# Kernel optimization log

Measured on AMD Instinct MI355X. Metric: run time of the kernel, lower is better.

The kernel has to match this reference:

```python
import jax, jax.numpy as jnp
import numpy as np

N = 8192      # batched tree nodes
HD = 1024     # head_dim
D = 1024      # input_dim == output_dim


def _xavier(key, shape):
    fan_out, fan_in = shape
    std = (2.0 / (fan_in + fan_out)) ** 0.5
    return std * jax.random.normal(key, shape, dtype=jnp.float32)


def setup_inputs() -> dict:
    key = jax.random.key(0)
    ks = jax.random.split(key, 16)
    inp = {
        "x_l": jax.random.normal(ks[0], (N, HD), jnp.float32),
        "h_l": jax.random.normal(ks[1], (N, D), jnp.float32),
        "c_l": jax.random.normal(ks[2], (N, D), jnp.float32),
        "x_r": jax.random.normal(ks[3], (N, HD), jnp.float32),
        "h_r": jax.random.normal(ks[4], (N, D), jnp.float32),
        "c_r": jax.random.normal(ks[5], (N, D), jnp.float32),
        # Linear weights stored torch-style [out, in]; biases init to 0 per reset_parameters
        "W_i": _xavier(ks[6], (D, 4 * D)),   "b_i": jnp.zeros((D,), jnp.float32),
        "W_fl": _xavier(ks[7], (D, 4 * D)),  "b_fl": jnp.zeros((D,), jnp.float32),
        "W_fr": _xavier(ks[8], (D, 4 * D)),  "b_fr": jnp.zeros((D,), jnp.float32),
        "W_xin": _xavier(ks[9], (4 * D, HD)),
        "W_o": _xavier(ks[10], (D, 3 * D)),  "b_o": jnp.zeros((D,), jnp.float32),
        "W_z": _xavier(ks[11], (HD, 2 * HD)), "b_z": jnp.zeros((HD,), jnp.float32),
        "W_g": _xavier(ks[12], (D, 2 * D)),  "b_g": jnp.zeros((D,), jnp.float32),
        "dim": 1,
    }
    return inp


def reference(x_l, h_l, c_l, x_r, h_r, c_r,
              W_i, b_i, W_fl, b_fl, W_fr, b_fr, W_xin,
              W_o, b_o, W_z, b_z, W_g, b_g, dim):
    lin = lambda x, W, b: x @ W.T + b
    # gating to merge child head representations
    child_x = jnp.concatenate([x_l, x_r], axis=dim)
    z_t = jax.nn.sigmoid(lin(child_x, W_z, b_z))
    x_t = z_t * x_l + (1.0 - z_t) * x_r
    # input projection (no bias), split into 4 gates
    x_in_t = x_t @ W_xin.T                      # [N, 4D]
    x_i, x_f, x_o, x_g = jnp.split(x_in_t, 4, axis=dim)
    concat_input = jnp.concatenate([h_l, h_r, c_l, c_r], axis=dim)  # [N, 4D]
    i_t = jax.nn.sigmoid(lin(concat_input, W_i, b_i) + x_i)
    f_lt = jax.nn.sigmoid(lin(concat_input, W_fl, b_fl) + x_f)
    f_rt = jax.nn.sigmoid(lin(concat_input, W_fr, b_fr) + x_f)
    concat_g = jnp.concatenate([h_l, h_r], axis=dim)
    g_t = jnp.tanh(x_g + lin(concat_g, W_g, b_g))  # dropout p=0 -> identity
    c_t = f_lt * c_l + f_rt * c_r + i_t * g_t
    concat_o = jnp.concatenate([h_l, h_r, c_t], axis=dim)
    o_t = jax.nn.sigmoid(x_o + lin(concat_o, W_o, b_o))
    h_t = o_t * jnp.tanh(c_t)
    return (x_t, h_t, c_t)
```

## Files before the change

### kernel.cpp

```cpp
#include <hip/hip_runtime.h>
#include <math.h>

#define NROWS 8192

typedef __attribute__((ext_vector_type(4))) float f32x4;
typedef __attribute__((ext_vector_type(4))) int i32x4;

__device__ __forceinline__ unsigned short f2bf(float f) {
  union { float f; unsigned int u; } v; v.f = f;
  unsigned int u = v.u;
  unsigned int r = (u + 0x7fffu + ((u >> 16) & 1u)) >> 16;
  return (unsigned short)r;
}
__device__ __forceinline__ float bf2f(unsigned short h) {
  union { unsigned int u; float f; } v; v.u = ((unsigned int)h) << 16;
  return v.f;
}
__device__ __forceinline__ float sigmoidf_(float x) { return 1.0f / (1.0f + expf(-x)); }

#define SA_INV   21.1666667f
#define SW3_INV  1016.0f
#define SWZ_INV  793.75f
#define SC_PRE3  4.64876e-5f
#define SC_ZG    5.95201e-5f

__device__ __forceinline__ unsigned char q8(float x, float inv) {
  float v = fminf(fmaxf(x * inv, -127.f), 127.f);
  return (unsigned char)(signed char)(int)rintf(v);
}

#define FENCE __builtin_amdgcn_sched_barrier(0)
#define BAR   __builtin_amdgcn_s_barrier()
#define WAIT_VM4  do { asm volatile("s_waitcnt vmcnt(4)" ::: "memory"); } while (0)
#define WAIT_VM0  do { asm volatile("s_waitcnt vmcnt(0)" ::: "memory"); } while (0)

#define LA8(buf, h) (((buf) * 4 + (h)) * 16384)
#define LB8(buf, h) (((buf) * 4 + 2 + (h)) * 16384)

#define GEMM_CORE8                                                              \
  __shared__ unsigned char lds8[131072];                                        \
  const int tid  = threadIdx.x;                                                 \
  const int wave = tid >> 6;                                                    \
  const int lane = tid & 63;                                                    \
  const int wm = wave >> 2;                                                     \
  const int wn = wave & 3;                                                      \
  const int lr = lane & 15;                                                     \
  const int kq = lane >> 4;                                                     \
  const int rsub = lane >> 3;                                                   \
  const int usw  = (lane & 7) ^ rsub;                                           \
  const int swz = (bid & 7) * (nwg >> 3) + (bid >> 3);                          \
  const int brow = (swz / nbx) * 256;                                           \
  const int bcol = (swz % nbx) * 256;                                           \
  const int nkt = K >> 7;                                                       \
  const int niter = K >> 8;                                                     \
  i32x4 acc[8][4];                                                              \
  _Pragma("unroll")                                                             \
  for (int m = 0; m < 8; ++m)                                                   \
    _Pragma("unroll")                                                           \
    for (int n = 0; n < 4; ++n)                                                 \
      acc[m][n] = (i32x4){0, 0, 0, 0};                                          \
  auto STAGE = [&](const unsigned char* src, int ld, int rowbase, int base_b,   \
                   int kt) {                                                    \
    const int k0 = (kt < nkt) ? (kt << 7) : 0;                                  \
    _Pragma("unroll")                                                           \
    for (int j = 0; j < 2; ++j) {                                               \
      const int chunk = wave * 2 + j;                                           \
      const unsigned char* g =                                                  \
          src + (size_t)(rowbase + chunk * 8 + rsub) * ld + k0 + usw * 16;      \
      __builtin_amdgcn_global_load_lds(                                         \
          (const __attribute__((address_space(1))) void*)g,                     \
          (__attribute__((address_space(3))) void*)&lds8[base_b + chunk * 1024],\
          16, 0, 0);                                                            \
    }                                                                           \
  };                                                                            \
  i32x4 aM[8], aM2[8], bN[4];                                                   \
  auto LDA_ = [&](int buf, int mh, i32x4* d) {                                  \
    _Pragma("unroll")                                                           \
    for (int m = 0; m < 4; ++m)                                                 \
      _Pragma("unroll")                                                         \
      for (int kk = 0; kk < 2; ++kk) {                                          \
        const int r = mh * 64 + m * 16 + lr;                                    \
        const int u = (kk * 4 + kq) ^ (lr & 7);                                 \
        d[m * 2 + kk] = *(const i32x4*)&lds8[LA8(buf, wm) + r * 128 + u * 16];  \
      }                                                                         \
  };                                                                            \
  auto LDB_ = [&](int buf, int nh, i32x4* d) {                                  \
    _Pragma("unroll")                                                           \
    for (int n = 0; n < 2; ++n)                                                 \
      _Pragma("unroll")                                                         \
      for (int kk = 0; kk < 2; ++kk) {                                          \
        const int r = (wn & 1) * 64 + nh * 32 + n * 16 + lr;                    \
        const int u = (kk * 4 + kq) ^ (lr & 7);                                 \
        d[n * 2 + kk] =                                                         \
            *(const i32x4*)&lds8[LB8(buf, wn >> 1) + r * 128 + u * 16];         \
      }                                                                         \
  };                                                                            \
  auto MM_ = [&](int mh, int nh, i32x4* a, i32x4* b) {                          \
    _Pragma("unroll")                                                           \
    for (int m = 0; m < 4; ++m)                                                 \
      _Pragma("unroll")                                                         \
      for (int n = 0; n < 2; ++n)                                               \
        _Pragma("unroll")                                                       \
        for (int kk = 0; kk < 2; ++kk)                                          \
          acc[mh * 4 + m][nh * 2 + n] =                                         \
              __builtin_amdgcn_mfma_i32_16x16x64_i8(                            \
                  a[m * 2 + kk], b[n * 2 + kk], acc[mh * 4 + m][nh * 2 + n],    \
                  0, 0, 0);                                                     \
  };                                                                            \
  STAGE(A, lda, brow,       LA8(0, 0), 0);                                      \
  STAGE(A, lda, brow + 128, LA8(0, 1), 0);                                      \
  STAGE(B, ldb, bcol,       LB8(0, 0), 0);                                      \
  STAGE(B, ldb, bcol + 128, LB8(0, 1), 0);                                      \
  STAGE(A, lda, brow,       LA8(1, 0), 1);                                      \
  STAGE(A, lda, brow + 128, LA8(1, 1), 1);                                      \
  WAIT_VM4; FENCE; BAR;                                                         \
  for (int i = 0; i < niter; ++i) {                                             \
    const int t1 = 2 * i + 1, t2 = 2 * i + 2, t3 = 2 * i + 3;                   \
    LDB_(0, 0, bN); LDA_(0, 0, aM); LDA_(0, 1, aM2);                            \
    STAGE(B, ldb, bcol,       LB8(1, 0), t1);                                   \
    STAGE(B, ldb, bcol + 128, LB8(1, 1), t1);                                   \
    FENCE; BAR; FENCE;                                                          \
    __builtin_amdgcn_s_setprio(1);                                              \
    MM_(0, 0, aM, bN); MM_(1, 0, aM2, bN);                                      \
    __builtin_amdgcn_s_setprio(0);                                              \
    FENCE; BAR;                                                                 \
    LDB_(0, 1, bN);                                                             \
    STAGE(A, lda, brow,       LA8(0, 0), t2);                                   \
    STAGE(A, lda, brow + 128, LA8(0, 1), t2);                                   \
    FENCE; BAR; FENCE;                                                          \
    __builtin_amdgcn_s_setprio(1);                                              \
    MM_(0, 1, aM, bN); MM_(1, 1, aM2, bN);                                      \
    __builtin_amdgcn_s_setprio(0);                                              \
    WAIT_VM4; FENCE; BAR;                                                       \
    LDB_(1, 0, bN); LDA_(1, 0, aM); LDA_(1, 1, aM2);                            \
    STAGE(B, ldb, bcol,       LB8(0, 0), t2);                                   \
    STAGE(B, ldb, bcol + 128, LB8(0, 1), t2);                                   \
    FENCE; BAR; FENCE;                                                          \
    __builtin_amdgcn_s_setprio(1);                                              \
    MM_(0, 0, aM, bN); MM_(1, 0, aM2, bN);                                      \
    __builtin_amdgcn_s_setprio(0);                                              \
    FENCE; BAR;                                                                 \
    LDB_(1, 1, bN);                                                             \
    STAGE(A, lda, brow,       LA8(1, 0), t3);                                   \
    STAGE(A, lda, brow + 128, LA8(1, 1), t3);                                   \
    FENCE; BAR; FENCE;                                                          \
    __builtin_amdgcn_s_setprio(1);                                              \
    MM_(0, 1, aM, bN); MM_(1, 1, aM2, bN);                                      \
    __builtin_amdgcn_s_setprio(0);                                              \
    WAIT_VM4; FENCE; BAR;                                                       \
  }                                                                             \
  WAIT_VM0;                                                                     \
  const int crow0 = brow + wm * 128 + kq * 4;                                   \
  const int ccol0 = bcol + wn * 64 + lr;

__global__ __launch_bounds__(512) void gemm_ACg8(
    const unsigned char* __restrict__ A3i, const unsigned char* __restrict__ W3q,
    unsigned short* __restrict__ pre3,
    const unsigned char* __restrict__ Wgq, unsigned short* __restrict__ preg,
    const unsigned char* __restrict__ A1q, const unsigned char* __restrict__ WbZq,
    unsigned short* __restrict__ zpre)
{
  const int b = (int)blockIdx.x;
  const unsigned char* A;
  const unsigned char* B;
  unsigned short* Cb;
  int K, lda, ldb, ldc, nbx, nwg, bid;
  float cscale;
  if (b < 384) {
    A = A3i; B = W3q; Cb = pre3; K = 4096; lda = 4096; ldb = 4096; ldc = 3072;
    nbx = 12; nwg = 384; bid = b; cscale = SC_PRE3;
  } else if (b < 512) {
    A = A3i; B = Wgq; Cb = preg; K = 2048; lda = 4096; ldb = 2048; ldc = 1024;
    nbx = 4; nwg = 128; bid = b - 384; cscale = SC_ZG;
  } else {
    A = A1q; B = WbZq; Cb = zpre; K = 2048; lda = 2048; ldb = 2048; ldc = 1024;
    nbx = 4; nwg = 128; bid = b - 512; cscale = SC_ZG;
  }
  GEMM_CORE8
#pragma unroll
  for (int mi = 0; mi < 8; ++mi)
#pragma unroll
    for (int ni = 0; ni < 4; ++ni)
#pragma unroll
      for (int j = 0; j < 4; ++j)
        Cb[(size_t)(crow0 + mi * 16 + j) * ldc + ccol0 + ni * 16] =
            f2bf((float)acc[mi][ni][j] * cscale);
}

__global__ __launch_bounds__(512) void gemm_B8(
    const unsigned char* __restrict__ A2q, const unsigned char* __restrict__ Wxq,
    unsigned short* __restrict__ xin)
{
  const int K = 1024, lda = 1024, ldb = 1024, ldc = 4096, nbx = 16;
  const int nwg = (int)gridDim.x;
  const int bid = (int)blockIdx.x;
  const unsigned char* A = A2q;
  const unsigned char* B = Wxq;
  GEMM_CORE8
#pragma unroll
  for (int mi = 0; mi < 8; ++mi)
#pragma unroll
    for (int ni = 0; ni < 4; ++ni)
#pragma unroll
      for (int j = 0; j < 4; ++j)
        xin[(size_t)(crow0 + mi * 16 + j) * ldc + ccol0 + ni * 16] =
            f2bf((float)acc[mi][ni][j] * SC_PRE3);
}

__global__ __launch_bounds__(512) void gemm_D8(
    const unsigned char* __restrict__ A3i, const unsigned char* __restrict__ Woq,
    unsigned short* __restrict__ opre0, unsigned short* __restrict__ opre1)
{
  const int b = (int)blockIdx.x;
  const bool sec = (b >= 128);
  const unsigned char* A = A3i + (sec ? 1536 : 0);
  const unsigned char* B = Woq + (sec ? 1536 : 0);
  unsigned short* Cb = sec ? opre1 : opre0;
  const int K = 1536, lda = 4096, ldb = 3072, ldc = 1024, nbx = 4, nwg = 128;
  const int bid = sec ? b - 128 : b;
  GEMM_CORE8
#pragma unroll
  for (int mi = 0; mi < 8; ++mi)
#pragma unroll
    for (int ni = 0; ni < 4; ++ni)
#pragma unroll
      for (int j = 0; j < 4; ++j)
        Cb[(size_t)(crow0 + mi * 16 + j) * ldc + ccol0 + ni * 16] =
            f2bf((float)acc[mi][ni][j] * SC_ZG);
}

#define NB_WZ 2048
#define NB_W3 12288
#define NB_WG 2048
#define NB_A1 16384
#define NB_A3 32768

__global__ void prep_kernel(unsigned char* __restrict__ WbZq, const float* __restrict__ W_z,
                            unsigned char* __restrict__ W3q,
                            const float* __restrict__ Wi, const float* __restrict__ Wfl,
                            const float* __restrict__ Wfr,
                            unsigned char* __restrict__ Wgq, const float* __restrict__ Wg,
                            unsigned char* __restrict__ A1q,
                            const float* __restrict__ x_l, const float* __restrict__ x_r,
                            unsigned short* __restrict__ Ac,
                            unsigned char* __restrict__ A3i,
                            const float* __restrict__ h_l, const float* __restrict__ h_r,
                            const float* __restrict__ c_l, const float* __restrict__ c_r)
{
  int b = (int)blockIdx.x;
  if (b < NB_WZ) {
    size_t idx = ((size_t)b * 256 + threadIdx.x) * 4;
    float4 v = *(const float4*)&W_z[idx];
    uchar4 q;
    q.x = q8(v.x, SWZ_INV); q.y = q8(v.y, SWZ_INV);
    q.z = q8(v.z, SWZ_INV); q.w = q8(v.w, SWZ_INV);
    *(uchar4*)&WbZq[idx] = q;
  } else if (b < NB_WZ + NB_W3) {
    size_t idx = ((size_t)(b - NB_WZ) * 256 + threadIdx.x) * 4;
    int m = (int)(idx >> 12);
    int k = (int)(idx & 4095);
    const float* W = (m < 1024) ? Wi : (m < 2048) ? Wfl : Wfr;
    float4 v = *(const float4*)&W[(size_t)(m & 1023) * 4096 + k];
    uchar4 q;
    q.x = q8(v.x, SW3_INV); q.y = q8(v.y, SW3_INV);
    q.z = q8(v.z, SW3_INV); q.w = q8(v.w, SW3_INV);
    *(uchar4*)&W3q[idx] = q;
  } else if (b < NB_WZ + NB_W3 + NB_WG) {
    size_t idx = ((size_t)(b - NB_WZ - NB_W3) * 256 + threadIdx.x) * 4;
    float4 v = *(const float4*)&Wg[idx];
    uchar4 q;
    q.x = q8(v.x, SWZ_INV); q.y = q8(v.y, SWZ_INV);
    q.z = q8(v.z, SWZ_INV); q.w = q8(v.w, SWZ_INV);
    *(uchar4*)&Wgq[idx] = q;
  } else if (b < NB_WZ + NB_W3 + NB_WG + NB_A1) {
    size_t idx = ((size_t)(b - NB_WZ - NB_W3 - NB_WG) * 256 + threadIdx.x) * 4;
    size_t n = idx >> 11;
    int rem = (int)(idx & 2047);
    const float* s = (rem < 1024) ? x_l : x_r;
    float4 v = *(const float4*)&s[(n << 10) + (rem & 1023)];
    uchar4 q;
    q.x = q8(v.x, SA_INV); q.y = q8(v.y, SA_INV);
    q.z = q8(v.z, SA_INV); q.w = q8(v.w, SA_INV);
    *(uchar4*)&A1q[idx] = q;
  } else {
    size_t idx = ((size_t)(b - NB_WZ - NB_W3 - NB_WG - NB_A1) * 256 + threadIdx.x) * 4;
    size_t n = idx >> 12;
    int rem = (int)(idx & 4095);
    int i = rem >> 10;
    int j = rem & 1023;
    const float* s = (i == 0) ? h_l : (i == 1) ? h_r : (i == 2) ? c_l : c_r;
    float4 v = *(const float4*)&s[(n << 10) + j];
    uchar4 q;
    q.x = q8(v.x, SA_INV); q.y = q8(v.y, SA_INV);
    q.z = q8(v.z, SA_INV); q.w = q8(v.w, SA_INV);
    *(uchar4*)&A3i[idx] = q;
    if (i >= 2) {
      ushort4 o;
      o.x = f2bf(v.x); o.y = f2bf(v.y); o.z = f2bf(v.z); o.w = f2bf(v.w);
      *(ushort4*)&Ac[n * 2048 + (i - 2) * 1024 + j] = o;
    }
  }
}

#define NB_EW1 8192
__global__ void ew1wx_kernel(const unsigned short* __restrict__ zp,
                             const float* __restrict__ bz,
                             const float* __restrict__ xl, const float* __restrict__ xr,
                             float* __restrict__ out_x, unsigned char* __restrict__ A2q,
                             unsigned char* __restrict__ Wxq, const float* __restrict__ W_xin)
{
  int b = (int)blockIdx.x;
  if (b < NB_EW1) {
    size_t idx = ((size_t)b * 256 + threadIdx.x) * 4;
    int j = (int)(idx & 1023);
    ushort4 z4 = *(const ushort4*)&zp[idx];
    float4 bz4 = *(const float4*)&bz[j];
    float4 xl4 = *(const float4*)&xl[idx];
    float4 xr4 = *(const float4*)&xr[idx];
    float4 xo;
    uchar4 aq;
    float z, xt;
    z = sigmoidf_(bf2f(z4.x) + bz4.x); xt = z * xl4.x + (1.f - z) * xr4.x; xo.x = xt; aq.x = q8(xt, SA_INV);
    z = sigmoidf_(bf2f(z4.y) + bz4.y); xt = z * xl4.y + (1.f - z) * xr4.y; xo.y = xt; aq.y = q8(xt, SA_INV);
    z = sigmoidf_(bf2f(z4.z) + bz4.z); xt = z * xl4.z + (1.f - z) * xr4.z; xo.z = xt; aq.z = q8(xt, SA_INV);
    z = sigmoidf_(bf2f(z4.w) + bz4.w); xt = z * xl4.w + (1.f - z) * xr4.w; xo.w = xt; aq.w = q8(xt, SA_INV);
    *(float4*)&out_x[idx] = xo;
    *(uchar4*)&A2q[idx] = aq;
  } else {
    size_t idx = ((size_t)(b - NB_EW1) * 256 + threadIdx.x) * 4;
    float4 v = *(const float4*)&W_xin[idx];
    uchar4 q;
    q.x = q8(v.x, SW3_INV); q.y = q8(v.y, SW3_INV);
    q.z = q8(v.z, SW3_INV); q.w = q8(v.w, SW3_INV);
    *(uchar4*)&Wxq[idx] = q;
  }
}

#define NB_EW2 8192
__global__ void ew2wo_kernel(const unsigned short* __restrict__ pre3,
                             const unsigned short* __restrict__ preg,
                             const unsigned short* __restrict__ xin,
                             const float* __restrict__ b_i, const float* __restrict__ b_fl,
                             const float* __restrict__ b_fr, const float* __restrict__ b_g,
                             float* __restrict__ out_c, unsigned short* __restrict__ Ac,
                             unsigned char* __restrict__ A3i,
                             unsigned char* __restrict__ Woq, const float* __restrict__ W_o)
{
  int b = (int)blockIdx.x;
  if (b < NB_EW2) {
    size_t idx = ((size_t)b * 256 + threadIdx.x) * 4;
    int j = (int)(idx & 1023);
    size_t n = idx >> 10;
    size_t r3 = n * 3072;
    size_t r4 = n << 12;
    size_t r2 = n << 11;
    ushort4 pi = *(const ushort4*)&pre3[r3 + j];
    ushort4 pf1 = *(const ushort4*)&pre3[r3 + 1024 + j];
    ushort4 pf2 = *(const ushort4*)&pre3[r3 + 2048 + j];
    ushort4 pg = *(const ushort4*)&preg[idx];
    ushort4 xi = *(const ushort4*)&xin[r4 + j];
    ushort4 xf = *(const ushort4*)&xin[r4 + 1024 + j];
    ushort4 xg = *(const ushort4*)&xin[r4 + 3072 + j];
    ushort4 cl4 = *(const ushort4*)&Ac[r2 + j];
    ushort4 cr4 = *(const ushort4*)&Ac[r2 + 1024 + j];
    float4 bi4 = *(const float4*)&b_i[j];
    float4 bfl4 = *(const float4*)&b_fl[j];
    float4 bfr4 = *(const float4*)&b_fr[j];
    float4 bg4 = *(const float4*)&b_g[j];
    float4 co;
    ushort4 ao;
    uchar4 aq;
#define EW2_ONE(pi_, pf1_, pf2_, pg_, xi_, xf_, xg_, bi_, bfl_, bfr_, bg_, cl_, cr_, oc_, oa_, oq_) \
    { float xiv = bf2f(xi_), xfv = bf2f(xf_), xgv = bf2f(xg_);                                      \
      float it = sigmoidf_(bf2f(pi_) + bi_ + xiv);                                                  \
      float fl = sigmoidf_(bf2f(pf1_) + bfl_ + xfv);                                                \
      float fr = sigmoidf_(bf2f(pf2_) + bfr_ + xfv);                                                \
      float g  = tanhf(bf2f(pg_) + bg_ + xgv);                                                      \
      float c_ = fl * bf2f(cl_) + fr * bf2f(cr_) + it * g;                                          \
      oc_ = c_; oa_ = f2bf(c_); oq_ = q8(c_, SA_INV); }
    EW2_ONE(pi.x, pf1.x, pf2.x, pg.x, xi.x, xf.x, xg.x, bi4.x, bfl4.x, bfr4.x, bg4.x, cl4.x, cr4.x, co.x, ao.x, aq.x)
    EW2_ONE(pi.y, pf1.y, pf2.y, pg.y, xi.y, xf.y, xg.y, bi4.y, bfl4.y, bfr4.y, bg4.y, cl4.y, cr4.y, co.y, ao.y, aq.y)
    EW2_ONE(pi.z, pf1.z, pf2.z, pg.z, xi.z, xf.z, xg.z, bi4.z, bfl4.z, bfr4.z, bg4.z, cl4.z, cr4.z, co.z, ao.z, aq.z)
    EW2_ONE(pi.w, pf1.w, pf2.w, pg.w, xi.w, xf.w, xg.w, bi4.w, bfl4.w, bfr4.w, bg4.w, cl4.w, cr4.w, co.w, ao.w, aq.w)
#undef EW2_ONE
    *(float4*)&out_c[idx] = co;
    *(ushort4*)&Ac[r2 + j] = ao;
    *(uchar4*)&A3i[r4 + 2048 + j] = aq;
  } else {
    size_t idx = ((size_t)(b - NB_EW2) * 256 + threadIdx.x) * 4;
    float4 v = *(const float4*)&W_o[idx];
    uchar4 q;
    q.x = q8(v.x, SWZ_INV); q.y = q8(v.y, SWZ_INV);
    q.z = q8(v.z, SWZ_INV); q.w = q8(v.w, SWZ_INV);
    *(uchar4*)&Woq[idx] = q;
  }
}

__global__ void ew3_kernel(const unsigned short* __restrict__ op0,
                           const unsigned short* __restrict__ op1,
                           const float* __restrict__ b_o,
                           const unsigned short* __restrict__ xin,
                           const unsigned short* __restrict__ Ac,
                           float* __restrict__ out_h)
{
  size_t idx = ((size_t)blockIdx.x * 256 + threadIdx.x) * 4;
  int j = (int)(idx & 1023);
  size_t n = idx >> 10;
  ushort4 opa = *(const ushort4*)&op0[idx];
  ushort4 opb = *(const ushort4*)&op1[idx];
  ushort4 xo = *(const ushort4*)&xin[(n << 12) + 2048 + j];
  ushort4 ct4 = *(const ushort4*)&Ac[(n << 11) + j];
  float4 bo4 = *(const float4*)&b_o[j];
  float4 ho;
  ho.x = sigmoidf_(bf2f(opa.x) + bf2f(opb.x) + bo4.x + bf2f(xo.x)) * tanhf(bf2f(ct4.x));
  ho.y = sigmoidf_(bf2f(opa.y) + bf2f(opb.y) + bo4.y + bf2f(xo.y)) * tanhf(bf2f(ct4.y));
  ho.z = sigmoidf_(bf2f(opa.z) + bf2f(opb.z) + bo4.z + bf2f(xo.z)) * tanhf(bf2f(ct4.z));
  ho.w = sigmoidf_(bf2f(opa.w) + bf2f(opb.w) + bo4.w + bf2f(xo.w)) * tanhf(bf2f(ct4.w));
  *(float4*)&out_h[idx] = ho;
}

extern "C" void kernel_launch(void* const* d_in, const int* in_sizes, int n_in,
                              void* d_out, int out_size, void* d_ws, size_t ws_size,
                              hipStream_t stream)
{
  const float* x_l  = (const float*)d_in[0];
  const float* h_l  = (const float*)d_in[1];
  const float* c_l  = (const float*)d_in[2];
  const float* x_r  = (const float*)d_in[3];
  const float* h_r  = (const float*)d_in[4];
  const float* c_r  = (const float*)d_in[5];
  const float* W_i  = (const float*)d_in[6];
  const float* b_i  = (const float*)d_in[7];
  const float* W_fl = (const float*)d_in[8];
  const float* b_fl = (const float*)d_in[9];
  const float* W_fr = (const float*)d_in[10];
  const float* b_fr = (const float*)d_in[11];
  const float* W_xin= (const float*)d_in[12];
  const float* W_o  = (const float*)d_in[13];
  const float* b_o  = (const float*)d_in[14];
  const float* W_z  = (const float*)d_in[15];
  const float* b_z  = (const float*)d_in[16];
  const float* W_g  = (const float*)d_in[17];
  const float* b_g  = (const float*)d_in[18];

  float* out_x = (float*)d_out;
  float* out_h = out_x + (size_t)NROWS * 1024;
  float* out_c = out_x + 2 * (size_t)NROWS * 1024;

  char* ws = (char*)d_ws;
  unsigned char*  A1q  = (unsigned char*)ws;
  unsigned short* xin  = (unsigned short*)ws;
  unsigned char*  A3i  = (unsigned char*)(ws + 67108864);
  unsigned short* Ac   = (unsigned short*)(ws + 100663296);
  unsigned short* zpre = (unsigned short*)(ws + 134217728);
  unsigned char*  Woq  = (unsigned char*)(ws + 134217728);
  unsigned char*  WbZq = (unsigned char*)(ws + 150994944);
  unsigned char*  W3q  = (unsigned char*)(ws + 153092096);
  unsigned char*  Wgq  = (unsigned char*)(ws + 165675008);
  unsigned char*  A2q  = (unsigned char*)(ws + 150994944);
  unsigned char*  Wxq  = (unsigned char*)(ws + 159383552);
  unsigned short* opre0= (unsigned short*)(ws + 150994944);
  unsigned short* preg = (unsigned short*)(ws + 167772160);
  unsigned short* opre1= (unsigned short*)(ws + 167772160);
  unsigned short* pre3 = (unsigned short*)(ws + 184549376);

  const dim3 blk(256);
  const dim3 gblk(512);

  prep_kernel<<<dim3(NB_WZ + NB_W3 + NB_WG + NB_A1 + NB_A3), blk, 0, stream>>>(
      WbZq, W_z, W3q, W_i, W_fl, W_fr, Wgq, W_g, A1q, x_l, x_r,
      Ac, A3i, h_l, h_r, c_l, c_r);

  gemm_ACg8<<<dim3(640), gblk, 0, stream>>>(A3i, W3q, pre3, Wgq, preg, A1q, WbZq, zpre);

  ew1wx_kernel<<<dim3(NB_EW1 + 4096), blk, 0, stream>>>(
      zpre, b_z, x_l, x_r, out_x, A2q, Wxq, W_xin);

  gemm_B8<<<dim3(512), gblk, 0, stream>>>(A2q, Wxq, xin);

  ew2wo_kernel<<<dim3(NB_EW2 + 3072), blk, 0, stream>>>(
      pre3, preg, xin, b_i, b_fl, b_fr, b_g, out_c, Ac, A3i, Woq, W_o);

  gemm_D8<<<dim3(256), gblk, 0, stream>>>(A3i, Woq, opre0, opre1);

  ew3_kernel<<<dim3(NB_EW1), blk, 0, stream>>>(opre0, opre1, b_o, xin, Ac, out_h);
}
```

Baseline: 351.8 us.

## Shrink int8 GEMM tiles to 128x128 with 256 threads and drop split-K in output GEMM

Changes all int8 MFMA GEMMs from 256x256 tiles with 512 threads and 128KB LDS to 128x128 tiles with 256 threads, 64KB LDS and launch bounds allowing two blocks per CU. Grid sizes grow by four times. The output-gate GEMM no longer splits K into two halves written to separate buffers; it runs the full K=3072 in one pass, so the final elementwise kernel reads one partial sum instead of two. The aim is better occupancy and wave overlap, at the cost of less data reuse per tile and more global/L2 traffic.

```diff
diff --git a/kernel.cpp b/kernel.cpp
--- a/kernel.cpp
+++ b/kernel.cpp
@@ -34,28 +34,28 @@
 #define WAIT_VM4  do { asm volatile("s_waitcnt vmcnt(4)" ::: "memory"); } while (0)
 #define WAIT_VM0  do { asm volatile("s_waitcnt vmcnt(0)" ::: "memory"); } while (0)
 
-#define LA8(buf, h) (((buf) * 4 + (h)) * 16384)
-#define LB8(buf, h) (((buf) * 4 + 2 + (h)) * 16384)
+#define LA8(buf) ((buf) * 32768)
+#define LB8(buf) ((buf) * 32768 + 16384)
 
 #define GEMM_CORE8                                                              \
-  __shared__ unsigned char lds8[131072];                                        \
+  __shared__ unsigned char lds8[65536];                                         \
   const int tid  = threadIdx.x;                                                 \
   const int wave = tid >> 6;                                                    \
   const int lane = tid & 63;                                                    \
-  const int wm = wave >> 2;                                                     \
-  const int wn = wave & 3;                                                      \
+  const int wm = wave >> 1;                                                     \
+  const int wn = wave & 1;                                                      \
   const int lr = lane & 15;                                                     \
   const int kq = lane >> 4;                                                     \
   const int rsub = lane >> 3;                                                   \
   const int usw  = (lane & 7) ^ rsub;                                           \
   const int swz = (bid & 7) * (nwg >> 3) + (bid >> 3);                          \
-  const int brow = (swz / nbx) * 256;                                           \
-  const int bcol = (swz % nbx) * 256;                                           \
+  const int brow = (swz / nbx) * 128;                                           \
+  const int bcol = (swz % nbx) * 128;                                           \
   const int nkt = K >> 7;                                                       \
   const int niter = K >> 8;                                                     \
-  i32x4 acc[8][4];                                                              \
+  i32x4 acc[4][4];                                                              \
   _Pragma("unroll")                                                             \
-  for (int m = 0; m < 8; ++m)                                                   \
+  for (int m = 0; m < 4; ++m)                                                   \
     _Pragma("unroll")                                                           \
     for (int n = 0; n < 4; ++n)                                                 \
       acc[m][n] = (i32x4){0, 0, 0, 0};                                          \
@@ -63,8 +63,8 @@
                    int kt) {                                                    \
     const int k0 = (kt < nkt) ? (kt << 7) : 0;                                  \
     _Pragma("unroll")                                                           \
-    for (int j = 0; j < 2; ++j) {                                               \
-      const int chunk = wave * 2 + j;                                           \
+    for (int j = 0; j < 4; ++j) {                                               \
+      const int chunk = wave * 4 + j;                                           \
       const unsigned char* g =                                                  \
           src + (size_t)(rowbase + chunk * 8 + rsub) * ld + k0 + usw * 16;      \
       __builtin_amdgcn_global_load_lds(                                         \
@@ -73,15 +73,15 @@
           16, 0, 0);                                                            \
     }                                                                           \
   };                                                                            \
-  i32x4 aM[8], aM2[8], bN[4];                                                   \
-  auto LDA_ = [&](int buf, int mh, i32x4* d) {                                  \
+  i32x4 aM[8], bN[4];                                                           \
+  auto LDA_ = [&](int buf, i32x4* d) {                                          \
     _Pragma("unroll")                                                           \
     for (int m = 0; m < 4; ++m)                                                 \
       _Pragma("unroll")                                                         \
       for (int kk = 0; kk < 2; ++kk) {                                          \
-        const int r = mh * 64 + m * 16 + lr;                                    \
+        const int r = wm * 64 + m * 16 + lr;                                    \
         const int u = (kk * 4 + kq) ^ (lr & 7);                                 \
-        d[m * 2 + kk] = *(const i32x4*)&lds8[LA8(buf, wm) + r * 128 + u * 16];  \
+        d[m * 2 + kk] = *(const i32x4*)&lds8[LA8(buf) + r * 128 + u * 16];      \
       }                                                                         \
   };                                                                            \
   auto LDB_ = [&](int buf, int nh, i32x4* d) {                                  \
@@ -89,71 +89,62 @@
     for (int n = 0; n < 2; ++n)                                                 \
       _Pragma("unroll")                                                         \
       for (int kk = 0; kk < 2; ++kk) {                                          \
-        const int r = (wn & 1) * 64 + nh * 32 + n * 16 + lr;                    \
+        const int r = wn * 64 + nh * 32 + n * 16 + lr;                          \
         const int u = (kk * 4 + kq) ^ (lr & 7);                                 \
-        d[n * 2 + kk] =                                                         \
-            *(const i32x4*)&lds8[LB8(buf, wn >> 1) + r * 128 + u * 16];         \
+        d[n * 2 + kk] = *(const i32x4*)&lds8[LB8(buf) + r * 128 + u * 16];      \
       }                                                                         \
   };                                                                            \
-  auto MM_ = [&](int mh, int nh, i32x4* a, i32x4* b) {                          \
+  auto MM_ = [&](int nh, i32x4* a, i32x4* b) {                                  \
     _Pragma("unroll")                                                           \
     for (int m = 0; m < 4; ++m)                                                 \
       _Pragma("unroll")                                                         \
       for (int n = 0; n < 2; ++n)                                               \
         _Pragma("unroll")                                                       \
         for (int kk = 0; kk < 2; ++kk)                                          \
-          acc[mh * 4 + m][nh * 2 + n] =                                         \
+          acc[m][nh * 2 + n] =                                                  \
               __builtin_amdgcn_mfma_i32_16x16x64_i8(                            \
-                  a[m * 2 + kk], b[n * 2 + kk], acc[mh * 4 + m][nh * 2 + n],    \
-                  0, 0, 0);                                                     \
+                  a[m * 2 + kk], b[n * 2 + kk], acc[m][nh * 2 + n], 0, 0, 0);   \
   };                                                                            \
-  STAGE(A, lda, brow,       LA8(0, 0), 0);                                      \
-  STAGE(A, lda, brow + 128, LA8(0, 1), 0);                                      \
-  STAGE(B, ldb, bcol,       LB8(0, 0), 0);                                      \
-  STAGE(B, ldb, bcol + 128, LB8(0, 1), 0);                                      \
-  STAGE(A, lda, brow,       LA8(1, 0), 1);                                      \
-  STAGE(A, lda, brow + 128, LA8(1, 1), 1);                                      \
+  STAGE(A, lda, brow, LA8(0), 0);                                               \
+  STAGE(B, ldb, bcol, LB8(0), 0);                                               \
+  STAGE(A, lda, brow, LA8(1), 1);                                               \
   WAIT_VM4; FENCE; BAR;                                                         \
   for (int i = 0; i < niter; ++i) {                                             \
     const int t1 = 2 * i + 1, t2 = 2 * i + 2, t3 = 2 * i + 3;                   \
-    LDB_(0, 0, bN); LDA_(0, 0, aM); LDA_(0, 1, aM2);                            \
-    STAGE(B, ldb, bcol,       LB8(1, 0), t1);                                   \
-    STAGE(B, ldb, bcol + 128, LB8(1, 1), t1);                                   \
+                             \
+    LDB_(0, 0, bN); LDA_(0, aM);                                                \
+    STAGE(B, ldb, bcol, LB8(1), t1);                                            \
     FENCE; BAR; FENCE;                                                          \
-    __builtin_amdgcn_s_setprio(1);                                              \
-    MM_(0, 0, aM, bN); MM_(1, 0, aM2, bN);                                      \
+    __builtin_amdgcn_s_setprio(1); MM_(0, aM, bN);                              \
     __builtin_amdgcn_s_setprio(0);                                              \
     FENCE; BAR;                                                                 \
+                      \
     LDB_(0, 1, bN);                                                             \
-    STAGE(A, lda, brow,       LA8(0, 0), t2);                                   \
-    STAGE(A, lda, brow + 128, LA8(0, 1), t2);                                   \
+    STAGE(A, lda, brow, LA8(0), t2);                                            \
     FENCE; BAR; FENCE;                                                          \
-    __builtin_amdgcn_s_setprio(1);                                              \
-    MM_(0, 1, aM, bN); MM_(1, 1, aM2, bN);                                      \
+    __builtin_amdgcn_s_setprio(1); MM_(1, aM, bN);                              \
     __builtin_amdgcn_s_setprio(0);                                              \
     WAIT_VM4; FENCE; BAR;                                                       \
-    LDB_(1, 0, bN); LDA_(1, 0, aM); LDA_(1, 1, aM2);                            \
-    STAGE(B, ldb, bcol,       LB8(0, 0), t2);                                   \
-    STAGE(B, ldb, bcol + 128, LB8(0, 1), t2);                                   \
+                                          \
+    LDB_(1, 0, bN); LDA_(1, aM);                                                \
+    STAGE(B, ldb, bcol, LB8(0), t2);                                            \
     FENCE; BAR; FENCE;                                                          \
-    __builtin_amdgcn_s_setprio(1);                                              \
-    MM_(0, 0, aM, bN); MM_(1, 0, aM2, bN);                                      \
+    __builtin_amdgcn_s_setprio(1); MM_(0, aM, bN);                              \
     __builtin_amdgcn_s_setprio(0);                                              \
     FENCE; BAR;                                                                 \
+                   \
     LDB_(1, 1, bN);                                                             \
-    STAGE(A, lda, brow,       LA8(1, 0), t3);                                   \
-    STAGE(A, lda, brow + 128, LA8(1, 1), t3);                                   \
+    STAGE(A, lda, brow, LA8(1), t3);                                            \
     FENCE; BAR; FENCE;                                                          \
-    __builtin_amdgcn_s_setprio(1);                                              \
-    MM_(0, 1, aM, bN); MM_(1, 1, aM2, bN);                                      \
+    __builtin_amdgcn_s_setprio(1); MM_(1, aM, bN);                              \
     __builtin_amdgcn_s_setprio(0);                                              \
     WAIT_VM4; FENCE; BAR;                                                       \
   }                                                                             \
   WAIT_VM0;                                                                     \
-  const int crow0 = brow + wm * 128 + kq * 4;                                   \
+  const int crow0 = brow + wm * 64 + kq * 4;                                    \
   const int ccol0 = bcol + wn * 64 + lr;
 
-__global__ __launch_bounds__(512) void gemm_ACg8(
+__global__ __launch_bounds__(256, 2) void gemm_ACg8(
     const unsigned char* __restrict__ A3i, const unsigned char* __restrict__ W3q,
     unsigned short* __restrict__ pre3,
     const unsigned char* __restrict__ Wgq, unsigned short* __restrict__ preg,
@@ -166,19 +157,19 @@
   unsigned short* Cb;
   int K, lda, ldb, ldc, nbx, nwg, bid;
   float cscale;
-  if (b < 384) {
+  if (b < 1536) {
     A = A3i; B = W3q; Cb = pre3; K = 4096; lda = 4096; ldb = 4096; ldc = 3072;
-    nbx = 12; nwg = 384; bid = b; cscale = SC_PRE3;
-  } else if (b < 512) {
+    nbx = 24; nwg = 1536; bid = b; cscale = SC_PRE3;
+  } else if (b < 2048) {
     A = A3i; B = Wgq; Cb = preg; K = 2048; lda = 4096; ldb = 2048; ldc = 1024;
-    nbx = 4; nwg = 128; bid = b - 384; cscale = SC_ZG;
+    nbx = 8; nwg = 512; bid = b - 1536; cscale = SC_ZG;
   } else {
     A = A1q; B = WbZq; Cb = zpre; K = 2048; lda = 2048; ldb = 2048; ldc = 1024;
-    nbx = 4; nwg = 128; bid = b - 512; cscale = SC_ZG;
+    nbx = 8; nwg = 512; bid = b - 2048; cscale = SC_ZG;
   }
   GEMM_CORE8
 #pragma unroll
-  for (int mi = 0; mi < 8; ++mi)
+  for (int mi = 0; mi < 4; ++mi)
 #pragma unroll
     for (int ni = 0; ni < 4; ++ni)
 #pragma unroll
@@ -187,18 +178,18 @@
             f2bf((float)acc[mi][ni][j] * cscale);
 }
 
-__global__ __launch_bounds__(512) void gemm_B8(
+__global__ __launch_bounds__(256, 2) void gemm_B8(
     const unsigned char* __restrict__ A2q, const unsigned char* __restrict__ Wxq,
     unsigned short* __restrict__ xin)
 {
-  const int K = 1024, lda = 1024, ldb = 1024, ldc = 4096, nbx = 16;
+  const int K = 1024, lda = 1024, ldb = 1024, ldc = 4096, nbx = 32;
   const int nwg = (int)gridDim.x;
   const int bid = (int)blockIdx.x;
   const unsigned char* A = A2q;
   const unsigned char* B = Wxq;
   GEMM_CORE8
 #pragma unroll
-  for (int mi = 0; mi < 8; ++mi)
+  for (int mi = 0; mi < 4; ++mi)
 #pragma unroll
     for (int ni = 0; ni < 4; ++ni)
 #pragma unroll
@@ -207,25 +198,23 @@
             f2bf((float)acc[mi][ni][j] * SC_PRE3);
 }
 
-__global__ __launch_bounds__(512) void gemm_D8(
+__global__ __launch_bounds__(256, 2) void gemm_D8(
     const unsigned char* __restrict__ A3i, const unsigned char* __restrict__ Woq,
-    unsigned short* __restrict__ opre0, unsigned short* __restrict__ opre1)
-{
-  const int b = (int)blockIdx.x;
-  const bool sec = (b >= 128);
-  const unsigned char* A = A3i + (sec ? 1536 : 0);
-  const unsigned char* B = Woq + (sec ? 1536 : 0);
-  unsigned short* Cb = sec ? opre1 : opre0;
-  const int K = 1536, lda = 4096, ldb = 3072, ldc = 1024, nbx = 4, nwg = 128;
-  const int bid = sec ? b - 128 : b;
+    unsigned short* __restrict__ opre)
+{
+  const int K = 3072, lda = 4096, ldb = 3072, ldc = 1024, nbx = 8;
+  const int nwg = (int)gridDim.x;
+  const int bid = (int)blockIdx.x;
+  const unsigned char* A = A3i;
+  const unsigned char* B = Woq;
   GEMM_CORE8
 #pragma unroll
-  for (int mi = 0; mi < 8; ++mi)
+  for (int mi = 0; mi < 4; ++mi)
 #pragma unroll
     for (int ni = 0; ni < 4; ++ni)
 #pragma unroll
       for (int j = 0; j < 4; ++j)
-        Cb[(size_t)(crow0 + mi * 16 + j) * ldc + ccol0 + ni * 16] =
+        opre[(size_t)(crow0 + mi * 16 + j) * ldc + ccol0 + ni * 16] =
             f2bf((float)acc[mi][ni][j] * SC_ZG);
 }
 
@@ -396,8 +385,7 @@
   }
 }
 
-__global__ void ew3_kernel(const unsigned short* __restrict__ op0,
-                           const unsigned short* __restrict__ op1,
+__global__ void ew3_kernel(const unsigned short* __restrict__ opre,
                            const float* __restrict__ b_o,
                            const unsigned short* __restrict__ xin,
                            const unsigned short* __restrict__ Ac,
@@ -406,16 +394,15 @@
   size_t idx = ((size_t)blockIdx.x * 256 + threadIdx.x) * 4;
   int j = (int)(idx & 1023);
   size_t n = idx >> 10;
-  ushort4 opa = *(const ushort4*)&op0[idx];
-  ushort4 opb = *(const ushort4*)&op1[idx];
+  ushort4 op = *(const ushort4*)&opre[idx];
   ushort4 xo = *(const ushort4*)&xin[(n << 12) + 2048 + j];
   ushort4 ct4 = *(const ushort4*)&Ac[(n << 11) + j];
   float4 bo4 = *(const float4*)&b_o[j];
   float4 ho;
-  ho.x = sigmoidf_(bf2f(opa.x) + bf2f(opb.x) + bo4.x + bf2f(xo.x)) * tanhf(bf2f(ct4.x));
-  ho.y = sigmoidf_(bf2f(opa.y) + bf2f(opb.y) + bo4.y + bf2f(xo.y)) * tanhf(bf2f(ct4.y));
-  ho.z = sigmoidf_(bf2f(opa.z) + bf2f(opb.z) + bo4.z + bf2f(xo.z)) * tanhf(bf2f(ct4.z));
-  ho.w = sigmoidf_(bf2f(opa.w) + bf2f(opb.w) + bo4.w + bf2f(xo.w)) * tanhf(bf2f(ct4.w));
+  ho.x = sigmoidf_(bf2f(op.x) + bo4.x + bf2f(xo.x)) * tanhf(bf2f(ct4.x));
+  ho.y = sigmoidf_(bf2f(op.y) + bo4.y + bf2f(xo.y)) * tanhf(bf2f(ct4.y));
+  ho.z = sigmoidf_(bf2f(op.z) + bo4.z + bf2f(xo.z)) * tanhf(bf2f(ct4.z));
+  ho.w = sigmoidf_(bf2f(op.w) + bo4.w + bf2f(xo.w)) * tanhf(bf2f(ct4.w));
   *(float4*)&out_h[idx] = ho;
 }
 
@@ -459,29 +446,27 @@
   unsigned char*  Wgq  = (unsigned char*)(ws + 165675008);
   unsigned char*  A2q  = (unsigned char*)(ws + 150994944);
   unsigned char*  Wxq  = (unsigned char*)(ws + 159383552);
-  unsigned short* opre0= (unsigned short*)(ws + 150994944);
+  unsigned short* opre = (unsigned short*)(ws + 150994944);
   unsigned short* preg = (unsigned short*)(ws + 167772160);
-  unsigned short* opre1= (unsigned short*)(ws + 167772160);
   unsigned short* pre3 = (unsigned short*)(ws + 184549376);
 
   const dim3 blk(256);
-  const dim3 gblk(512);
 
   prep_kernel<<<dim3(NB_WZ + NB_W3 + NB_WG + NB_A1 + NB_A3), blk, 0, stream>>>(
       WbZq, W_z, W3q, W_i, W_fl, W_fr, Wgq, W_g, A1q, x_l, x_r,
       Ac, A3i, h_l, h_r, c_l, c_r);
 
-  gemm_ACg8<<<dim3(640), gblk, 0, stream>>>(A3i, W3q, pre3, Wgq, preg, A1q, WbZq, zpre);
+  gemm_ACg8<<<dim3(2560), blk, 0, stream>>>(A3i, W3q, pre3, Wgq, preg, A1q, WbZq, zpre);
 
   ew1wx_kernel<<<dim3(NB_EW1 + 4096), blk, 0, stream>>>(
       zpre, b_z, x_l, x_r, out_x, A2q, Wxq, W_xin);
 
-  gemm_B8<<<dim3(512), gblk, 0, stream>>>(A2q, Wxq, xin);
+  gemm_B8<<<dim3(2048), blk, 0, stream>>>(A2q, Wxq, xin);
 
   ew2wo_kernel<<<dim3(NB_EW2 + 3072), blk, 0, stream>>>(
       pre3, preg, xin, b_i, b_fl, b_fr, b_g, out_c, Ac, A3i, Woq, W_o);
 
-  gemm_D8<<<dim3(256), gblk, 0, stream>>>(A3i, Woq, opre0, opre1);
-
-  ew3_kernel<<<dim3(NB_EW1), blk, 0, stream>>>(opre0, opre1, b_o, xin, Ac, out_h);
-}
+  gemm_D8<<<dim3(512), blk, 0, stream>>>(A3i, Woq, opre);
+
+  ew3_kernel<<<dim3(NB_EW1), blk, 0, stream>>>(opre, b_o, xin, Ac, out_h);
+}
```

Measured after the change: 359.3 us. +2.1%, slower.
